# Kernel optimization log

Measured on AMD Instinct MI355X. Metric: run time of the kernel, lower is better.

Reference implementation:

```python
import jax, jax.numpy as jnp
import numpy as np
from jax import lax

BN_EPS = 1e-5


def _bn(t, g, b, m, v):
    # eval-mode BatchNorm2d over channel axis 1
    scale = (g / jnp.sqrt(v + BN_EPS))[None, :, None, None]
    return (t - m[None, :, None, None]) * scale + b[None, :, None, None]


def _conv1x1(t, w):
    # w: (out_c, in_c)
    return jnp.einsum('bchw,oc->bohw', t, w)


def setup_inputs() -> dict:
    key = jax.random.key(0)
    ks = jax.random.split(key, 8)
    B, C_in, H, W = 16, 640, 32, 32
    x = jax.random.normal(ks[0], (B, C_in, H, W), dtype=jnp.float32)

    def bn_params(k, c):
        k1, k2, k3, k4 = jax.random.split(k, 4)
        return (jax.random.normal(k1, (c,), jnp.float32) * 0.1 + 1.0,  # gamma
                jax.random.normal(k2, (c,), jnp.float32) * 0.1,        # beta
                jax.random.normal(k3, (c,), jnp.float32) * 0.1,        # running mean
                jax.random.uniform(k4, (c,), jnp.float32) + 0.5)       # running var

    bn1_g, bn1_b, bn1_m, bn1_v = bn_params(ks[1], 640)
    w_in = jax.random.normal(ks[2], (64, 640), jnp.float32) / np.sqrt(640)
    bnin_g, bnin_b, bnin_m, bnin_v = bn_params(ks[3], 64)
    w_emb = jax.random.normal(ks[4], (640, 1664), jnp.float32) / np.sqrt(1664)
    bne_g, bne_b, bne_m, bne_v = bn_params(ks[5], 640)
    w_out = jax.random.normal(ks[6], (640, 640), jnp.float32) / np.sqrt(640)
    bno_g, bno_b, bno_m, bno_v = bn_params(ks[7], 640)

    return dict(x=x,
                bn1_g=bn1_g, bn1_b=bn1_b, bn1_m=bn1_m, bn1_v=bn1_v,
                w_in=w_in, bnin_g=bnin_g, bnin_b=bnin_b, bnin_m=bnin_m, bnin_v=bnin_v,
                w_emb=w_emb, bne_g=bne_g, bne_b=bne_b, bne_m=bne_m, bne_v=bne_v,
                w_out=w_out, bno_g=bno_g, bno_b=bno_b, bno_m=bno_m, bno_v=bno_v)


def reference(x,
              bn1_g, bn1_b, bn1_m, bn1_v,
              w_in, bnin_g, bnin_b, bnin_m, bnin_v,
              w_emb, bne_g, bne_b, bne_m, bne_v,
              w_out, bno_g, bno_b, bno_m, bno_v):
    KH, KW = 5, 5
    x = jax.nn.relu(_bn(x, bn1_g, bn1_b, bn1_m, bn1_v))
    x = jax.nn.relu(_bn(_conv1x1(x, w_in), bnin_g, bnin_b, bnin_m, bnin_v))
    x0 = jax.nn.relu(x)  # second ReLU in original forward (no-op but faithful)
    # F.normalize(x, dim=1, p=2), eps=1e-12 (PyTorch default)
    norm = jnp.sqrt(jnp.sum(x0 * x0, axis=1, keepdims=True))
    identity = x0 / jnp.maximum(norm, 1e-12)
    b, c, h, w = identity.shape
    # unfold: (b, c*KH*KW, h, w), channel-major ordering matches torch Unfold
    patches = lax.conv_general_dilated_patches(
        identity, (KH, KW), (1, 1), ((2, 2), (2, 2)))
    corr = patches.reshape(b, c, KH * KW, h, w) * identity[:, :, None, :, :]
    corr = corr.reshape(b, c * KH * KW, h, w)
    # featureL2Norm: sqrt(sum(x^2, 1) + 1e-6)
    gs = corr / jnp.sqrt(jnp.sum(corr * corr, axis=1, keepdims=True) + 1e-6)
    feat = jnp.concatenate([identity, gs], axis=1)  # (b, 1664, h, w)
    e = jax.nn.relu(_bn(_conv1x1(feat, w_emb), bne_g, bne_b, bne_m, bne_v))
    out = _bn(_conv1x1(e, w_out), bno_g, bno_b, bno_m, bno_v)
    # dropout in eval mode = identity
    return out
```

## Files before the change

### kernel.cpp

```cpp
#include <hip/hip_runtime.h>
#include <math.h>

#define BN_EPS 1e-5f

using short8  = __attribute__((ext_vector_type(8))) short;
using f32x16  = __attribute__((ext_vector_type(16))) float;


__device__ __forceinline__ float bflo(unsigned u) { return __uint_as_float(u << 16); }
__device__ __forceinline__ float bfhi(unsigned u) { return __uint_as_float(u & 0xffff0000u); }

__device__ __forceinline__ unsigned bf16_rne(float f) {
    unsigned u = __float_as_uint(f);
    return (u + 0x7fffu + ((u >> 16) & 1u)) >> 16;
}
__device__ __forceinline__ unsigned pack_bf16(float lo, float hi) {
    return bf16_rne(lo) | (bf16_rne(hi) << 16);
}
__device__ __forceinline__ unsigned pk_hu(float lo, float hi) {
    unsigned a = __float_as_uint(lo) + 0x8000u;
    unsigned b = __float_as_uint(hi) + 0x8000u;
    return __builtin_amdgcn_perm(b, a, 0x07060302u);
}
__device__ __forceinline__ unsigned pmul_fast(unsigned a, unsigned b) {
    return pk_hu(bflo(a) * bflo(b), bfhi(a) * bfhi(b));
}

__global__ __launch_bounds__(256)
void k_prepAll(const float* __restrict__ g1, const float* __restrict__ b1,
               const float* __restrict__ m1, const float* __restrict__ v1,
               const float* __restrict__ w_in,
               const float* __restrict__ gi, const float* __restrict__ bi,
               const float* __restrict__ mi, const float* __restrict__ vi,
               const float* __restrict__ w_emb,
               const float* __restrict__ ge, const float* __restrict__ be,
               const float* __restrict__ me, const float* __restrict__ ve,
               const float* __restrict__ w_out,
               const float* __restrict__ go, const float* __restrict__ bo,
               const float* __restrict__ mo, const float* __restrict__ vo,
               float* __restrict__ s1, float* __restrict__ b1c,
               float* __restrict__ biasI, float* __restrict__ biasE, float* __restrict__ biasO,
               unsigned* __restrict__ wIt, unsigned* __restrict__ wEt, unsigned* __restrict__ wOt)
{
    __shared__ float row[1664];
    const int tid = threadIdx.x;

    if (blockIdx.x < 640) {
        const int oc = blockIdx.x;
#pragma unroll
        for (int it = 0; it < 2; it++) {
            int u = it * 256 + tid;
            if (u < 416)
                ((float4*)row)[u] = ((const float4*)&w_emb[(size_t)oc * 1664])[u];
        }
        __syncthreads();
        if (tid < 208) {
            int kc = tid >> 2, kh = (tid >> 1) & 1, ksub = tid & 1;
            int k0 = kc * 32 + kh * 16 + ksub * 8;
            float sc = ge[oc] * rsqrtf(ve[oc] + BN_EPS);
            float v[8];
#pragma unroll
            for (int j = 0; j < 8; j++) {
                int kgp = k0 + j;
                int orig;
                if (kgp < 64) orig = kgp;
                else { int t = kgp - 64; orig = 64 + (t & 63) * 25 + (t >> 6); }
                v[j] = row[orig] * sc;
            }
            int mt = oc >> 7, mf = (oc >> 5) & 3;
            int idx = (mt * 52 + kc) * 512 + (mf * 2 + kh) * 64 + ksub * 32 + (oc & 31);
            ((uint4*)wEt)[idx] = make_uint4(pack_bf16(v[0], v[1]), pack_bf16(v[2], v[3]),
                                            pack_bf16(v[4], v[5]), pack_bf16(v[6], v[7]));
        }
        return;
    }

    int i = (blockIdx.x - 640) * 256 + tid;

    if (i < 640) {
        float s = g1[i] * rsqrtf(v1[i] + BN_EPS);
        s1[i] = s; b1c[i] = b1[i] - m1[i] * s;
    } else if (i < 704) {
        int c = i - 640;
        float s = gi[c] * rsqrtf(vi[c] + BN_EPS);
        biasI[c] = bi[c] - mi[c] * s;
    } else if (i < 1344) {
        int c = i - 704;
        float s = ge[c] * rsqrtf(ve[c] + BN_EPS);
        biasE[c] = be[c] - me[c] * s;
    } else if (i < 1984) {
        int c = i - 1344;
        float s = go[c] * rsqrtf(vo[c] + BN_EPS);
        biasO[c] = bo[c] - mo[c] * s;
    }

    if (i >= 2048 && i < 7168) {
        int u = i - 2048;
        int kc = u >> 8, w = u & 255;
        int mf = w >> 7, kh = (w >> 6) & 1, sl = w & 63;
        int oc = mf * 32 + (sl & 31);
        int k0 = kc * 32 + kh * 16 + (sl >> 5) * 8;
        float sc = gi[oc] * rsqrtf(vi[oc] + BN_EPS);
        unsigned d[4];
#pragma unroll
        for (int q = 0; q < 4; q++)
            d[q] = pack_bf16(w_in[oc * 640 + k0 + 2 * q] * sc,
                             w_in[oc * 640 + k0 + 2 * q + 1] * sc);
        ((uint4*)wIt)[u] = make_uint4(d[0], d[1], d[2], d[3]);
    }

    if (i >= 8192 && i < 59392) {
        int u = i - 8192;
        int ci = u >> 9, w = u & 511;
        int mt = ci / 20, kc = ci - mt * 20;
        int mf = w >> 7, kh = (w >> 6) & 1, sl = w & 63;
        int oc = mt * 128 + mf * 32 + (sl & 31);
        int k0 = kc * 32 + kh * 16 + (sl >> 5) * 8;
        float sc = go[oc] * rsqrtf(vo[oc] + BN_EPS);
        unsigned d[4];
#pragma unroll
        for (int q = 0; q < 4; q++)
            d[q] = pack_bf16(w_out[oc * 640 + k0 + 2 * q] * sc,
                             w_out[oc * 640 + k0 + 2 * q + 1] * sc);
        ((uint4*)wOt)[u] = make_uint4(d[0], d[1], d[2], d[3]);
    }
}

__global__ __launch_bounds__(512, 1)
void k_identity(const float* __restrict__ x,
                const float* __restrict__ s1, const float* __restrict__ b1c,
                const unsigned* __restrict__ wIt, const float* __restrict__ biasI,
                unsigned* __restrict__ ident)
{
    __shared__ short smem[2][4096];
    __shared__ float Tpart[64 * 65];
    __shared__ float T[64 * 68];
    __shared__ float inv[64];

    const int tid  = threadIdx.x;
    const int half = tid >> 8;
    const int t    = tid & 255;
    const int l = t & 63, wv = t >> 6;
    const int mf = wv >> 1, nf = wv & 1;
    const int p0 = blockIdx.x * 64;
    const int b = p0 >> 10, hw0 = p0 & 1023;

    f32x16 acc;
#pragma unroll
    for (int r = 0; r < 16; r++) acc[r] = 0.f;

    for (int i = 0; i < 10; i++) {
        const int kc = half * 10 + i;
        uint4 av = ((const uint4*)wIt)[kc * 256 + t];
        int bnf = t >> 7, bkh = (t >> 6) & 1, sl = t & 63;
        int px = bnf * 32 + (sl & 31);
        int ch0 = kc * 32 + bkh * 16 + (sl >> 5) * 8;
        float4 sA = *(const float4*)&s1[ch0], sB = *(const float4*)&s1[ch0 + 4];
        float4 bA = *(const float4*)&b1c[ch0], bB = *(const float4*)&b1c[ch0 + 4];
        float vv[8];
        const float* xp = &x[((size_t)b * 640 + ch0) * 1024 + hw0 + px];
        vv[0] = fmaxf(fmaf(xp[0], sA.x, bA.x), 0.f);
        vv[1] = fmaxf(fmaf(xp[1024], sA.y, bA.y), 0.f);
        vv[2] = fmaxf(fmaf(xp[2048], sA.z, bA.z), 0.f);
        vv[3] = fmaxf(fmaf(xp[3072], sA.w, bA.w), 0.f);
        vv[4] = fmaxf(fmaf(xp[4096], sB.x, bB.x), 0.f);
        vv[5] = fmaxf(fmaf(xp[5120], sB.y, bB.y), 0.f);
        vv[6] = fmaxf(fmaf(xp[6144], sB.z, bB.z), 0.f);
        vv[7] = fmaxf(fmaf(xp[7168], sB.w, bB.w), 0.f);
        uint4 bvpk = make_uint4(pack_bf16(vv[0], vv[1]), pack_bf16(vv[2], vv[3]),
                                pack_bf16(vv[4], vv[5]), pack_bf16(vv[6], vv[7]));
        __syncthreads();
        ((uint4*)smem[half])[t] = av;
        ((uint4*)(smem[half] + 2048))[t] = bvpk;
        __syncthreads();
#pragma unroll
        for (int kh = 0; kh < 2; kh++) {
            short8 a  = *(const short8*)&smem[half][((mf * 2 + kh) * 64 + l) * 8];
            short8 bb = *(const short8*)&smem[half][2048 + ((nf * 2 + kh) * 64 + l) * 8];
            acc = __builtin_amdgcn_mfma_f32_32x32x16_bf16(a, bb, acc, 0, 0, 0);
        }
    }
    if (half == 1) {
#pragma unroll
        for (int r = 0; r < 16; r++) {
            int m = mf * 32 + (r & 3) + 8 * (r >> 2) + 4 * (l >> 5);
            int px = nf * 32 + (l & 31);
            Tpart[px * 65 + m] = acc[r];
        }
    }
    __syncthreads();
    if (half == 0) {
#pragma unroll
        for (int r = 0; r < 16; r++) {
            int m = mf * 32 + (r & 3) + 8 * (r >> 2) + 4 * (l >> 5);
            int px = nf * 32 + (l & 31);
            float v = acc[r] + Tpart[px * 65 + m];
            T[px * 68 + m] = fmaxf(v + biasI[m], 0.f);
        }
    }
    __syncthreads();
    if (tid < 64) {
        float sum = 0.f;
#pragma unroll 8
        for (int c = 0; c < 64; c++) { float v = T[tid * 68 + c]; sum = fmaf(v, v, sum); }
        inv[tid] = 1.f / fmaxf(sqrtf(sum), 1e-12f);
    }
    __syncthreads();
    {
        int px = tid >> 3, q = tid & 7;
        float iv = inv[px];
        unsigned d[4];
#pragma unroll
        for (int t2 = 0; t2 < 4; t2++)
            d[t2] = pack_bf16(T[px * 68 + q * 8 + 2 * t2] * iv,
                              T[px * 68 + q * 8 + 2 * t2 + 1] * iv);
        *(uint4*)&ident[(size_t)(p0 + px) * 32 + q * 4] = make_uint4(d[0], d[1], d[2], d[3]);
    }
}

#define FS_SLAB 0
#define FS_CTRS 15552
__global__ __launch_bounds__(512, 1)
void k_feat(const unsigned* __restrict__ ident, unsigned* __restrict__ featC, int ptBase)
{
    __shared__ short smem[20160];
    __shared__ float invDs[64];

    const int tid = threadIdx.x;
    const int pt = ptBase + blockIdx.x;
    const int b = pt >> 4, r0 = (pt & 15) * 2;

#pragma unroll
    for (int it = 0; it < 4; it++) {
        int u = it * 512 + tid;
        if (u < 1728) {
            int spx = u >> 3, q = u & 7;
            int sr = spx / 36, sc = spx - sr * 36;
            int r = r0 + sr - 2, c = sc - 2;
            uint4 v = make_uint4(0u, 0u, 0u, 0u);
            if (r >= 0 && r < 32 && c >= 0 && c < 32)
                v = *(const uint4*)&ident[((size_t)(b * 1024 + r * 32 + c) * 64 + q * 8) / 2];
            *(uint4*)&smem[FS_SLAB + spx * 72 + q * 8] = v;
        }
    }
    __syncthreads();

    {
        int px = tid >> 3, part = tid & 7;
        int rh = px >> 5, rw = px & 31;
        float ctr[8];
        const unsigned* cp = (const unsigned*)&smem[FS_SLAB + ((rh + 2) * 36 + rw + 2) * 72 + part * 8];
#pragma unroll
        for (int d = 0; d < 4; d++) { ctr[2 * d] = bflo(cp[d]); ctr[2 * d + 1] = bfhi(cp[d]); }
        float sum = 0.f;
#pragma unroll
        for (int k = 0; k < 25; k++) {
            const int kh = k / 5, kw = k % 5;
            const unsigned* nb = (const unsigned*)&smem[FS_SLAB + ((rh + kh) * 36 + rw + kw) * 72 + part * 8];
#pragma unroll
            for (int d = 0; d < 4; d++) {
                float q0 = bflo(nb[d]) * ctr[2 * d];
                float q1 = bfhi(nb[d]) * ctr[2 * d + 1];
                sum = fmaf(q0, q0, sum); sum = fmaf(q1, q1, sum);
            }
        }
        sum += __shfl_xor(sum, 1);
        sum += __shfl_xor(sum, 2);
        sum += __shfl_xor(sum, 4);
        if (part == 0) invDs[px] = rsqrtf(sum + 1e-6f);
    }
    __syncthreads();

    {
        int px = tid >> 3, q = tid & 7;
        int spx = ((px >> 5) + 2) * 36 + (px & 31) + 2;
        const unsigned* src = (const unsigned*)&smem[FS_SLAB + spx * 72 + q * 8];
        float iv = invDs[px];
        unsigned d[4];
#pragma unroll
        for (int dd = 0; dd < 4; dd++)
            d[dd] = pk_hu(bflo(src[dd]) * iv, bfhi(src[dd]) * iv);
        *(uint4*)&smem[FS_CTRS + px * 72 + q * 8] = make_uint4(d[0], d[1], d[2], d[3]);
    }
    __syncthreads();

    const int t = tid & 255;
    const int hf = t >> 7, bkh = (t >> 6) & 1, sl = t & 63;
    const int pxl = hf * 32 + (sl & 31);
    const int cl = bkh * 16 + (sl >> 5) * 8;
    const int spxC = (hf + 2) * 36 + (sl & 31) + 2;
    const int kcH = tid >> 8;
    uint4* dst = (uint4*)featC + (size_t)blockIdx.x * 52 * 256 + t;

    for (int it = 0; it < 26; it++) {
        int kc = it * 2 + kcH;
        uint4 f;
        if (kc < 2) {
            f = *(const uint4*)&smem[FS_SLAB + spxC * 72 + kc * 32 + cl];
        } else {
            int idx = kc - 2;
            int ksp = idx >> 1;
            int cb = (idx & 1) * 32 + cl;
            int kho = ksp / 5, kwo = ksp - kho * 5;
            int spx = (hf + kho) * 36 + (sl & 31) + kwo;
            const unsigned* nb = (const unsigned*)&smem[FS_SLAB + spx * 72 + cb];
            const unsigned* ct = (const unsigned*)&smem[FS_CTRS + pxl * 72 + cb];
            f = make_uint4(pmul_fast(nb[0], ct[0]), pmul_fast(nb[1], ct[1]),
                           pmul_fast(nb[2], ct[2]), pmul_fast(nb[3], ct[3]));
        }
        dst[kc * 256] = f;
    }
}

__global__ __launch_bounds__(640, 3)
void k_embout(const unsigned* __restrict__ featC, const unsigned* __restrict__ wEt,
              const float* __restrict__ biasE,
              const unsigned* __restrict__ wOt, const float* __restrict__ biasO,
              float* __restrict__ out, int ntBase)
{
    __shared__ char lds[2][16384];
    __shared__ uint4 Ep[20 * 256];

    const int tid = threadIdx.x;
    const int l = tid & 63;
    const int w = tid >> 6;
    const int mt = w >> 1, mf0 = (w & 1) * 2;
    const int ntL = blockIdx.x;

    const uint4* A = (const uint4*)wEt + (size_t)(mt * 52) * 512;
    const uint4* B = (const uint4*)featC + (size_t)ntL * 52 * 256;

    const int u0 = tid;
    const int u1 = tid + 640;
    const bool has2 = (tid < 384);

    f32x16 acc[2][2];
#pragma unroll
    for (int i = 0; i < 2; i++)
#pragma unroll
        for (int j = 0; j < 2; j++)
#pragma unroll
            for (int r = 0; r < 16; r++) acc[i][j][r] = 0.f;

    uint4 s0 = B[u0];
    uint4 s1;
    if (has2) s1 = B[u1];
    *(uint4*)&lds[0][u0 * 16] = s0;
    if (has2) *(uint4*)&lds[0][u1 * 16] = s1;
    __syncthreads();

    for (int c = 0; c < 13; c++) {
        const int cur = c & 1, nxt = cur ^ 1;
        if (c < 12) {
            s0 = B[(c + 1) * 1024 + u0];
            if (has2) s1 = B[(c + 1) * 1024 + u1];
        }
#pragma unroll
        for (int kcL = 0; kcL < 4; kcL++) {
            const int kc = c * 4 + kcL;
            uint4 av[2][2], bv[2][2];
#pragma unroll
            for (int mi = 0; mi < 2; mi++)
#pragma unroll
                for (int kh = 0; kh < 2; kh++)
                    av[mi][kh] = A[(size_t)kc * 512 + (((mf0 + mi) * 2 + kh) << 6) + l];
#pragma unroll
            for (int ni = 0; ni < 2; ni++)
#pragma unroll
                for (int kh = 0; kh < 2; kh++)
                    bv[ni][kh] = *(const uint4*)&lds[cur][(kcL * 256 + (ni << 7) + (kh << 6) + l) * 16];
#pragma unroll
            for (int kh = 0; kh < 2; kh++) {
                acc[0][0] = __builtin_amdgcn_mfma_f32_32x32x16_bf16(*(short8*)&av[0][kh], *(short8*)&bv[0][kh], acc[0][0], 0, 0, 0);
                acc[0][1] = __builtin_amdgcn_mfma_f32_32x32x16_bf16(*(short8*)&av[0][kh], *(short8*)&bv[1][kh], acc[0][1], 0, 0, 0);
                acc[1][0] = __builtin_amdgcn_mfma_f32_32x32x16_bf16(*(short8*)&av[1][kh], *(short8*)&bv[0][kh], acc[1][0], 0, 0, 0);
                acc[1][1] = __builtin_amdgcn_mfma_f32_32x32x16_bf16(*(short8*)&av[1][kh], *(short8*)&bv[1][kh], acc[1][1], 0, 0, 0);
            }
        }
        if (c < 12) {
            *(uint4*)&lds[nxt][u0 * 16] = s0;
            if (has2) *(uint4*)&lds[nxt][u1 * 16] = s1;
        }
        __syncthreads();
    }

#pragma unroll
    for (int mi = 0; mi < 2; mi++) {
        const int kbase = (w * 2 + mi) * 256;
#pragma unroll
        for (int ni = 0; ni < 2; ni++) {
#pragma unroll
            for (int rg = 0; rg < 4; rg++) {
                int ocb = w * 64 + mi * 32 + 8 * rg + 4 * (l >> 5);
                float4 bb = *(const float4*)&biasE[ocb];
                unsigned d0 = pack_bf16(fmaxf(acc[mi][ni][rg * 4 + 0] + bb.x, 0.f),
                                        fmaxf(acc[mi][ni][rg * 4 + 1] + bb.y, 0.f));
                unsigned d1 = pack_bf16(fmaxf(acc[mi][ni][rg * 4 + 2] + bb.z, 0.f),
                                        fmaxf(acc[mi][ni][rg * 4 + 3] + bb.w, 0.f));
                int unit = kbase + (ni << 7) + ((rg >> 1) << 6) + ((rg & 1) << 5) + (l & 31);
                ((uint2*)Ep)[unit * 2 + (l >> 5)] = make_uint2(d0, d1);
            }
        }
    }
    __syncthreads();

    const int nt = ntBase + ntL;
    const int p0 = nt * 64;
    const int b = p0 >> 10, hw0 = p0 & 1023;
    const uint4* Ao = (const uint4*)wOt + (size_t)(mt * 20) * 512;

    f32x16 acc2[2][2];
#pragma unroll
    for (int i = 0; i < 2; i++)
#pragma unroll
        for (int j = 0; j < 2; j++)
#pragma unroll
            for (int r = 0; r < 16; r++) acc2[i][j][r] = 0.f;

#pragma unroll 2
    for (int kc = 0; kc < 20; kc++) {
        uint4 av[2][2], bv[2][2];
#pragma unroll
        for (int mi = 0; mi < 2; mi++)
#pragma unroll
            for (int kh = 0; kh < 2; kh++)
                av[mi][kh] = Ao[(size_t)kc * 512 + (((mf0 + mi) * 2 + kh) << 6) + l];
#pragma unroll
        for (int ni = 0; ni < 2; ni++)
#pragma unroll
            for (int kh = 0; kh < 2; kh++)
                bv[ni][kh] = Ep[kc * 256 + (ni << 7) + (kh << 6) + l];
#pragma unroll
        for (int kh = 0; kh < 2; kh++) {
            acc2[0][0] = __builtin_amdgcn_mfma_f32_32x32x16_bf16(*(short8*)&av[0][kh], *(short8*)&bv[0][kh], acc2[0][0], 0, 0, 0);
            acc2[0][1] = __builtin_amdgcn_mfma_f32_32x32x16_bf16(*(short8*)&av[0][kh], *(short8*)&bv[1][kh], acc2[0][1], 0, 0, 0);
            acc2[1][0] = __builtin_amdgcn_mfma_f32_32x32x16_bf16(*(short8*)&av[1][kh], *(short8*)&bv[0][kh], acc2[1][0], 0, 0, 0);
            acc2[1][1] = __builtin_amdgcn_mfma_f32_32x32x16_bf16(*(short8*)&av[1][kh], *(short8*)&bv[1][kh], acc2[1][1], 0, 0, 0);
        }
    }

#pragma unroll
    for (int mi = 0; mi < 2; mi++)
#pragma unroll
        for (int ni = 0; ni < 2; ni++) {
            int pxl = ni * 32 + (l & 31);
#pragma unroll
            for (int r = 0; r < 16; r++) {
                int oc = w * 64 + mi * 32 + (r & 3) + 8 * (r >> 2) + 4 * (l >> 5);
                out[((size_t)b * 640 + oc) * 1024 + hw0 + pxl] = acc2[mi][ni][r] + biasO[oc];
            }
        }
}

extern "C" void kernel_launch(void* const* d_in, const int* in_sizes, int n_in,
                              void* d_out, int out_size, void* d_ws, size_t ws_size,
                              hipStream_t stream)
{
    const float* x    = (const float*)d_in[0];
    const float* g1   = (const float*)d_in[1];
    const float* b1   = (const float*)d_in[2];
    const float* m1   = (const float*)d_in[3];
    const float* v1   = (const float*)d_in[4];
    const float* w_in = (const float*)d_in[5];
    const float* gi   = (const float*)d_in[6];
    const float* bi   = (const float*)d_in[7];
    const float* mi   = (const float*)d_in[8];
    const float* vi   = (const float*)d_in[9];
    const float* w_emb= (const float*)d_in[10];
    const float* ge   = (const float*)d_in[11];
    const float* be   = (const float*)d_in[12];
    const float* me   = (const float*)d_in[13];
    const float* ve   = (const float*)d_in[14];
    const float* w_out= (const float*)d_in[15];
    const float* go   = (const float*)d_in[16];
    const float* bo   = (const float*)d_in[17];
    const float* mo   = (const float*)d_in[18];
    const float* vo   = (const float*)d_in[19];

    char* ws = (char*)d_ws;
    float*    s1    = (float*)(ws + 0);
    float*    b1c   = (float*)(ws + 2560);
    float*    biasI = (float*)(ws + 5120);
    float*    biasE = (float*)(ws + 5376);
    float*    biasO = (float*)(ws + 7936);
    unsigned* wIt   = (unsigned*)(ws + 16384);
    unsigned* wOt   = (unsigned*)(ws + 98304);
    unsigned* wEt   = (unsigned*)(ws + 917504);
    unsigned* ident = (unsigned*)(ws + 3047424);
    unsigned* featC = (unsigned*)(ws + 5144576);
    float*    out   = (float*)d_out;

    const size_t featFullBytes = 256ull * 52 * 256 * 16;
    const size_t featFullEnd   = 5144576ull + featFullBytes;

    k_prepAll<<<872, 256, 0, stream>>>(g1, b1, m1, v1, w_in, gi, bi, mi, vi,
                                       w_emb, ge, be, me, ve, w_out, go, bo, mo, vo,
                                       s1, b1c, biasI, biasE, biasO, wIt, wEt, wOt);
    k_identity<<<256, 512, 0, stream>>>(x, s1, b1c, wIt, biasI, ident);

    if (ws_size >= featFullEnd) {
        k_feat<<<256, 512, 0, stream>>>(ident, featC, 0);
        k_embout<<<256, 640, 0, stream>>>(featC, wEt, biasE, wOt, biasO, out, 0);
    } else {
        for (int c = 0; c < 64; c++) {
            k_feat<<<4, 512, 0, stream>>>(ident, featC, c * 4);
            k_embout<<<4, 640, 0, stream>>>(featC, wEt, biasE, wOt, biasO, out, c * 4);
        }
    }
}
```

Baseline: 208.2 us.

## Fuse correlation feature generation into embedding GEMM kernel, dropping featC buffer

Merges k_feat into k_embout so each block builds its 5x5 correlation features in LDS and feeds them straight into the MFMA pipeline. The features are no longer written to and read back from a global featC buffer (about 54MB of traffic), and one launch is removed. In exchange LDS use per block grows (slab, ctrs and staging buffers) and launch bounds drop to 1 block per CU, which lowers occupancy. Feature generation now sits inside the GEMM loop rather than overlapping a global prefetch.

After: 195.6 us. -6.0%, faster.

```diff
diff --git a/kernel.cpp b/kernel.cpp
--- a/kernel.cpp
+++ b/kernel.cpp
@@ -218,45 +218,75 @@
     }
 }
 
-#define FS_SLAB 0
-#define FS_CTRS 15552
-__global__ __launch_bounds__(512, 1)
-void k_feat(const unsigned* __restrict__ ident, unsigned* __restrict__ featC, int ptBase)
+__device__ __forceinline__ uint4 gen_feat_unit(const short* slab, const short* ctrs,
+                                               int kcAbs, int t)
 {
-    __shared__ short smem[20160];
+    const int hf = t >> 7, sl = t & 63;
+    const int bkh = (t >> 6) & 1;
+    const int cl = bkh * 16 + (sl >> 5) * 8;
+    if (kcAbs < 2) {
+        int spxC = (hf + 2) * 36 + (sl & 31) + 2;
+        return *(const uint4*)&slab[spxC * 72 + kcAbs * 32 + cl];
+    } else {
+        int pxl = hf * 32 + (sl & 31);
+        int idx = kcAbs - 2;
+        int ksp = idx >> 1;
+        int cb = (idx & 1) * 32 + cl;
+        int kho = ksp / 5, kwo = ksp - kho * 5;
+        int spx = (hf + kho) * 36 + (sl & 31) + kwo;
+        const unsigned* nb = (const unsigned*)&slab[spx * 72 + cb];
+        const unsigned* ct = (const unsigned*)&ctrs[pxl * 72 + cb];
+        return make_uint4(pmul_fast(nb[0], ct[0]), pmul_fast(nb[1], ct[1]),
+                          pmul_fast(nb[2], ct[2]), pmul_fast(nb[3], ct[3]));
+    }
+}
+
+__global__ __launch_bounds__(640, 1)
+void k_fused(const unsigned* __restrict__ ident,
+             const unsigned* __restrict__ wEt, const float* __restrict__ biasE,
+             const unsigned* __restrict__ wOt, const float* __restrict__ biasO,
+             float* __restrict__ out)
+{
+    __shared__ short slab[15552];
+    __shared__ short ctrs[4608];
     __shared__ float invDs[64];
+    __shared__ char  stg[2][16384];
+    __shared__ uint4 Ep[20 * 256];
 
     const int tid = threadIdx.x;
-    const int pt = ptBase + blockIdx.x;
+    const int l = tid & 63;
+    const int w = tid >> 6;
+    const int mt = w >> 1, mf0 = (w & 1) * 2;
+    const int pt = blockIdx.x;
     const int b = pt >> 4, r0 = (pt & 15) * 2;
 
 #pragma unroll
-    for (int it = 0; it < 4; it++) {
-        int u = it * 512 + tid;
+    for (int it = 0; it < 3; it++) {
+        int u = it * 640 + tid;
         if (u < 1728) {
             int spx = u >> 3, q = u & 7;
             int sr = spx / 36, sc = spx - sr * 36;
-            int r = r0 + sr - 2, c = sc - 2;
+            int r = r0 + sr - 2, cc = sc - 2;
             uint4 v = make_uint4(0u, 0u, 0u, 0u);
-            if (r >= 0 && r < 32 && c >= 0 && c < 32)
-                v = *(const uint4*)&ident[((size_t)(b * 1024 + r * 32 + c) * 64 + q * 8) / 2];
-            *(uint4*)&smem[FS_SLAB + spx * 72 + q * 8] = v;
-        }
-    }
-    __syncthreads();
-
-    {
+            if (r >= 0 && r < 32 && cc >= 0 && cc < 32)
+                v = *(const uint4*)&ident[((size_t)(b * 1024 + r * 32 + cc) * 64 + q * 8) / 2];
+            *(uint4*)&slab[spx * 72 + q * 8] = v;
+        }
+    }
+    __syncthreads();
+
+    if (tid < 512) {
         int px = tid >> 3, part = tid & 7;
         int rh = px >> 5, rw = px & 31;
         float ctr[8];
-        const unsigned* cp = (const unsigned*)&smem[FS_SLAB + ((rh + 2) * 36 + rw + 2) * 72 + part * 8];
+        const unsigned* cp = (const unsigned*)&slab[((rh + 2) * 36 + rw + 2) * 72 + part * 8];
 #pragma unroll
         for (int d = 0; d < 4; d++) { ctr[2 * d] = bflo(cp[d]); ctr[2 * d + 1] = bfhi(cp[d]); }
         float sum = 0.f;
 #pragma unroll
         for (int k = 0; k < 25; k++) {
             const int kh = k / 5, kw = k % 5;
-            const unsigned* nb = (const unsigned*)&smem[FS_SLAB + ((rh + kh) * 36 + rw + kw) * 72 + part * 8];
+            const unsigned* nb = (const unsigned*)&slab[((rh + kh) * 36 + rw + kw) * 72 + part * 8];
 #pragma unroll
             for (int d = 0; d < 4; d++) {
                 float q0 = bflo(nb[d]) * ctr[2 * d];
@@ -271,67 +301,20 @@
     }
     __syncthreads();
 
-    {
+    if (tid < 512) {
         int px = tid >> 3, q = tid & 7;
         int spx = ((px >> 5) + 2) * 36 + (px & 31) + 2;
-        const unsigned* src = (const unsigned*)&smem[FS_SLAB + spx * 72 + q * 8];
+        const unsigned* src = (const unsigned*)&slab[spx * 72 + q * 8];
         float iv = invDs[px];
         unsigned d[4];
 #pragma unroll
         for (int dd = 0; dd < 4; dd++)
             d[dd] = pk_hu(bflo(src[dd]) * iv, bfhi(src[dd]) * iv);
-        *(uint4*)&smem[FS_CTRS + px * 72 + q * 8] = make_uint4(d[0], d[1], d[2], d[3]);
-    }
-    __syncthreads();
-
-    const int t = tid & 255;
-    const int hf = t >> 7, bkh = (t >> 6) & 1, sl = t & 63;
-    const int pxl = hf * 32 + (sl & 31);
-    const int cl = bkh * 16 + (sl >> 5) * 8;
-    const int spxC = (hf + 2) * 36 + (sl & 31) + 2;
-    const int kcH = tid >> 8;
-    uint4* dst = (uint4*)featC + (size_t)blockIdx.x * 52 * 256 + t;
-
-    for (int it = 0; it < 26; it++) {
-        int kc = it * 2 + kcH;
-        uint4 f;
-        if (kc < 2) {
-            f = *(const uint4*)&smem[FS_SLAB + spxC * 72 + kc * 32 + cl];
-        } else {
-            int idx = kc - 2;
-            int ksp = idx >> 1;
-            int cb = (idx & 1) * 32 + cl;
-            int kho = ksp / 5, kwo = ksp - kho * 5;
-            int spx = (hf + kho) * 36 + (sl & 31) + kwo;
-            const unsigned* nb = (const unsigned*)&smem[FS_SLAB + spx * 72 + cb];
-            const unsigned* ct = (const unsigned*)&smem[FS_CTRS + pxl * 72 + cb];
-            f = make_uint4(pmul_fast(nb[0], ct[0]), pmul_fast(nb[1], ct[1]),
-                           pmul_fast(nb[2], ct[2]), pmul_fast(nb[3], ct[3]));
-        }
-        dst[kc * 256] = f;
-    }
-}
-
-__global__ __launch_bounds__(640, 3)
-void k_embout(const unsigned* __restrict__ featC, const unsigned* __restrict__ wEt,
-              const float* __restrict__ biasE,
-              const unsigned* __restrict__ wOt, const float* __restrict__ biasO,
-              float* __restrict__ out, int ntBase)
-{
-    __shared__ char lds[2][16384];
-    __shared__ uint4 Ep[20 * 256];
-
-    const int tid = threadIdx.x;
-    const int l = tid & 63;
-    const int w = tid >> 6;
-    const int mt = w >> 1, mf0 = (w & 1) * 2;
-    const int ntL = blockIdx.x;
+        *(uint4*)&ctrs[px * 72 + q * 8] = make_uint4(d[0], d[1], d[2], d[3]);
+    }
+    __syncthreads();
 
     const uint4* A = (const uint4*)wEt + (size_t)(mt * 52) * 512;
-    const uint4* B = (const uint4*)featC + (size_t)ntL * 52 * 256;
-
-    const int u0 = tid;
-    const int u1 = tid + 640;
     const bool has2 = (tid < 384);
 
     f32x16 acc[2][2];
@@ -342,18 +325,28 @@
 #pragma unroll
             for (int r = 0; r < 16; r++) acc[i][j][r] = 0.f;
 
-    uint4 s0 = B[u0];
-    uint4 s1;
-    if (has2) s1 = B[u1];
-    *(uint4*)&lds[0][u0 * 16] = s0;
-    if (has2) *(uint4*)&lds[0][u1 * 16] = s1;
+    {
+        uint4 f = gen_feat_unit(slab, ctrs, (tid >> 8), tid & 255);
+        *(uint4*)&stg[0][tid * 16] = f;
+        if (has2) {
+            int u = tid + 640;
+            uint4 f2 = gen_feat_unit(slab, ctrs, (u >> 8), u & 255);
+            *(uint4*)&stg[0][u * 16] = f2;
+        }
+    }
     __syncthreads();
 
     for (int c = 0; c < 13; c++) {
         const int cur = c & 1, nxt = cur ^ 1;
         if (c < 12) {
-            s0 = B[(c + 1) * 1024 + u0];
-            if (has2) s1 = B[(c + 1) * 1024 + u1];
+            int kc0 = (c + 1) * 4;
+            uint4 f = gen_feat_unit(slab, ctrs, kc0 + (tid >> 8), tid & 255);
+            *(uint4*)&stg[nxt][tid * 16] = f;
+            if (has2) {
+                int u = tid + 640;
+                uint4 f2 = gen_feat_unit(slab, ctrs, kc0 + (u >> 8), u & 255);
+                *(uint4*)&stg[nxt][u * 16] = f2;
+            }
         }
 #pragma unroll
         for (int kcL = 0; kcL < 4; kcL++) {
@@ -368,7 +361,7 @@
             for (int ni = 0; ni < 2; ni++)
 #pragma unroll
                 for (int kh = 0; kh < 2; kh++)
-                    bv[ni][kh] = *(const uint4*)&lds[cur][(kcL * 256 + (ni << 7) + (kh << 6) + l) * 16];
+                    bv[ni][kh] = *(const uint4*)&stg[cur][(kcL * 256 + (ni << 7) + (kh << 6) + l) * 16];
 #pragma unroll
             for (int kh = 0; kh < 2; kh++) {
                 acc[0][0] = __builtin_amdgcn_mfma_f32_32x32x16_bf16(*(short8*)&av[0][kh], *(short8*)&bv[0][kh], acc[0][0], 0, 0, 0);
@@ -376,10 +369,6 @@
                 acc[1][0] = __builtin_amdgcn_mfma_f32_32x32x16_bf16(*(short8*)&av[1][kh], *(short8*)&bv[0][kh], acc[1][0], 0, 0, 0);
                 acc[1][1] = __builtin_amdgcn_mfma_f32_32x32x16_bf16(*(short8*)&av[1][kh], *(short8*)&bv[1][kh], acc[1][1], 0, 0, 0);
             }
-        }
-        if (c < 12) {
-            *(uint4*)&lds[nxt][u0 * 16] = s0;
-            if (has2) *(uint4*)&lds[nxt][u1 * 16] = s1;
         }
         __syncthreads();
     }
@@ -404,9 +393,8 @@
     }
     __syncthreads();
 
-    const int nt = ntBase + ntL;
-    const int p0 = nt * 64;
-    const int b = p0 >> 10, hw0 = p0 & 1023;
+    const int p0 = pt * 64;
+    const int hw0 = p0 & 1023;
     const uint4* Ao = (const uint4*)wOt + (size_t)(mt * 20) * 512;
 
     f32x16 acc2[2][2];
@@ -487,24 +475,11 @@
     unsigned* wOt   = (unsigned*)(ws + 98304);
     unsigned* wEt   = (unsigned*)(ws + 917504);
     unsigned* ident = (unsigned*)(ws + 3047424);
-    unsigned* featC = (unsigned*)(ws + 5144576);
     float*    out   = (float*)d_out;
-
-    const size_t featFullBytes = 256ull * 52 * 256 * 16;
-    const size_t featFullEnd   = 5144576ull + featFullBytes;
 
     k_prepAll<<<872, 256, 0, stream>>>(g1, b1, m1, v1, w_in, gi, bi, mi, vi,
                                        w_emb, ge, be, me, ve, w_out, go, bo, mo, vo,
                                        s1, b1c, biasI, biasE, biasO, wIt, wEt, wOt);
     k_identity<<<256, 512, 0, stream>>>(x, s1, b1c, wIt, biasI, ident);
-
-    if (ws_size >= featFullEnd) {
-        k_feat<<<256, 512, 0, stream>>>(ident, featC, 0);
-        k_embout<<<256, 640, 0, stream>>>(featC, wEt, biasE, wOt, biasO, out, 0);
-    } else {
-        for (int c = 0; c < 64; c++) {
-            k_feat<<<4, 512, 0, stream>>>(ident, featC, c * 4);
-            k_embout<<<4, 640, 0, stream>>>(featC, wEt, biasE, wOt, biasO, out, c * 4);
-        }
-    }
-}
+    k_fused<<<256, 640, 0, stream>>>(ident, wEt, biasE, wOt, biasO, out);
+}
```
